# Kernel optimization log

Hardware: AMD Instinct MI355X
Metric: run time of the kernel (lower is better)

Reference implementation:

```python
import jax, jax.numpy as jnp
import numpy as np

B = 4096  # number of rows (batch of 1-D sequences)
N = 4096  # transform length


def setup_inputs() -> dict:
    key = jax.random.key(0)
    x = jax.random.normal(key, (B, N), dtype=jnp.float32)
    # get_expk(N): expk[k] = (cos(pi*k/(2N)), -sin(pi*k/(2N)))
    t = jnp.arange(N, dtype=jnp.float32) * (np.pi / (2.0 * N))
    expk = jnp.stack([jnp.cos(t), -jnp.sin(t)], axis=-1)  # [N, 2]
    return {"x": x, "expk": expk}


def reference(x, expk):
    # IDCT (DCT-III), 2N-point FFT formulation:
    #   y_k = x_0 + 2 * sum_{n=1}^{N-1} x_n cos(pi*n*(2k+1)/(2N))
    #       = Re{ sum_n w_n x_n exp(j*pi*n/(2N)) * exp(j*2*pi*n*k/(2N)) },  w_0=1, w_n=2
    # i.e. the first N outputs of a 2N-point inverse DFT of the zero-padded,
    # twiddle-premultiplied sequence.
    n = x.shape[-1]
    # expk stores (cos(theta), -sin(theta)) => exp(+j*theta) = expk0 - j*expk1
    coef = (expk[..., 0] - 1j * expk[..., 1]).astype(jnp.complex64)  # [N]
    w = jnp.concatenate([jnp.ones((1,), x.dtype), jnp.full((n - 1,), 2.0, x.dtype)])
    a = (x * w).astype(jnp.complex64) * coef                      # [B, N]
    A = jnp.concatenate([a, jnp.zeros_like(a)], axis=-1)          # [B, 2N] zero-pad
    y = jnp.real(jnp.fft.ifft(A, axis=-1))[..., :n] * (2.0 * n)   # undo 1/(2N) of ifft
    return y.astype(x.dtype)
```

## Files before the change

### kernel.cpp

```cpp
#include <hip/hip_runtime.h>


#define NFFT 4096
#define NT   256
#define SWZ(p) ((p) ^ (((p) >> 3) & 0xE))

__device__ __forceinline__ void cmul(float ar, float ai, float br, float bi,
                                     float& orr, float& oii) {
    orr = ar * br - ai * bi;
    oii = ar * bi + ai * br;
}

__device__ __forceinline__ void dft16(float vr[16], float vi[16]) {
    constexpr float WR[4][4] = {
        {1.f, 1.f, 1.f, 1.f},
        {1.f,  0.92387953251128674f,  0.70710678118654752f,  0.38268343236508977f},
        {1.f,  0.70710678118654752f,  0.f,                  -0.70710678118654752f},
        {1.f,  0.38268343236508977f, -0.70710678118654752f, -0.92387953251128674f}};
    constexpr float WI[4][4] = {
        {0.f, 0.f, 0.f, 0.f},
        {0.f,  0.38268343236508977f,  0.70710678118654752f,  0.92387953251128674f},
        {0.f,  0.70710678118654752f,  1.f,                   0.70710678118654752f},
        {0.f,  0.92387953251128674f,  0.70710678118654752f, -0.38268343236508977f}};
    float ur[16], ui[16];
#pragma unroll
    for (int p = 0; p < 4; ++p) {
        float apcr = vr[p] + vr[p + 8],      apci = vi[p] + vi[p + 8];
        float amcr = vr[p] - vr[p + 8],      amci = vi[p] - vi[p + 8];
        float bpdr = vr[p + 4] + vr[p + 12], bpdi = vi[p + 4] + vi[p + 12];
        float bmdr = vr[p + 4] - vr[p + 12], bmdi = vi[p + 4] - vi[p + 12];
        float y0r = apcr + bpdr, y0i = apci + bpdi;
        float y1r = amcr - bmdi, y1i = amci + bmdr;
        float y2r = apcr - bpdr, y2i = apci - bpdi;
        float y3r = amcr + bmdi, y3i = amci - bmdr;
        ur[4 * p + 0] = y0r;  ui[4 * p + 0] = y0i;
        cmul(y1r, y1i, WR[p][1], WI[p][1], ur[4 * p + 1], ui[4 * p + 1]);
        cmul(y2r, y2i, WR[p][2], WI[p][2], ur[4 * p + 2], ui[4 * p + 2]);
        cmul(y3r, y3i, WR[p][3], WI[p][3], ur[4 * p + 3], ui[4 * p + 3]);
    }
#pragma unroll
    for (int q = 0; q < 4; ++q) {
        float apcr = ur[q] + ur[q + 8],      apci = ui[q] + ui[q + 8];
        float amcr = ur[q] - ur[q + 8],      amci = ui[q] - ui[q + 8];
        float bpdr = ur[q + 4] + ur[q + 12], bpdi = ui[q + 4] + ui[q + 12];
        float bmdr = ur[q + 4] - ur[q + 12], bmdi = ui[q + 4] - ui[q + 12];
        vr[q]      = apcr + bpdr;  vi[q]      = apci + bpdi;
        vr[q + 4]  = amcr - bmdi;  vi[q + 4]  = amci + bmdr;
        vr[q + 8]  = apcr - bpdr;  vi[q + 8]  = apci - bpdi;
        vr[q + 12] = amcr + bmdi;  vi[q + 12] = amci - bmdr;
    }
}

__device__ __forceinline__ void twiddle_apply(float vr[16], float vi[16],
                                              float w1r, float w1i) {
    float cr = w1r, ci = w1i;
#pragma unroll
    for (int r = 1; r < 16; ++r) {
        float tr, ti;
        cmul(vr[r], vi[r], cr, ci, tr, ti);
        vr[r] = tr; vi[r] = ti;
        if (r < 15) {
            float nr, ni;
            cmul(cr, ci, w1r, w1i, nr, ni);
            cr = nr; ci = ni;
        }
    }
}

extern "C" __global__ void __launch_bounds__(NT, 5)
idct_fft_kernel(const float* __restrict__ x, const float* __restrict__ expk,
                float* __restrict__ out)
{
    __shared__ __align__(16) float2 S[NFFT];
    float* __restrict__ Sf = (float*)S;

    const int tid = threadIdx.x;
    const long row = blockIdx.x;
    const float* __restrict__ xrow = x + row * (long)NFFT;
    const float2* __restrict__ e2 = (const float2*)expk;

    float vr[16], vi[16];
#pragma unroll
    for (int j = 0; j < 16; ++j) {
        int n = tid + NT * j;
        float xv = xrow[n];
        float2 e = e2[n];
        float w = (n == 0) ? 1.0f : 2.0f;
        vr[j] = w * xv * e.x;
        vi[j] = -(w * xv * e.y);
    }
    dft16(vr, vi);
    {
        float2 we = e2[4 * tid];
        twiddle_apply(vr, vi, we.x, -we.y);
    }
#pragma unroll
    for (int rp = 0; rp < 8; ++rp) {
        int p = 16 * tid + 2 * rp;
        float4 st = make_float4(vr[2 * rp], vi[2 * rp], vr[2 * rp + 1], vi[2 * rp + 1]);
        *(float4*)&S[SWZ(p)] = st;
    }
    __syncthreads();

#pragma unroll
    for (int j = 0; j < 16; ++j) {
        float2 c = S[SWZ(tid + NT * j)];
        vr[j] = c.x; vi[j] = c.y;
    }
    __syncthreads();
    dft16(vr, vi);
    {
        float2 we = e2[64 * (tid >> 4)];
        twiddle_apply(vr, vi, we.x, -we.y);
    }
    {
        int ba = (tid & 15) + ((tid >> 4) << 8);
#pragma unroll
        for (int r = 0; r < 16; ++r) {
            S[SWZ(ba + 16 * r)] = make_float2(vr[r], vi[r]);
        }
    }
    __syncthreads();

#pragma unroll
    for (int j = 0; j < 16; ++j) {
        float2 c = S[SWZ(tid + NT * j)];
        vr[j] = c.x; vi[j] = c.y;
    }
    __syncthreads();
    dft16(vr, vi);
#pragma unroll
    for (int r = 0; r < 16; ++r) {
        Sf[tid + NT * r] = vr[r];
    }
    __syncthreads();

    float2* __restrict__ y2 = (float2*)(out + row * (long)NFFT);
#pragma unroll
    for (int t = 0; t < 8; ++t) {
        int m = tid + NT * t;
        float a = Sf[m];
        float b = Sf[NFFT - 1 - m];
        y2[m] = make_float2(a, b);
    }
}

extern "C" void kernel_launch(void* const* d_in, const int* in_sizes, int n_in,
                              void* d_out, int out_size, void* d_ws, size_t ws_size,
                              hipStream_t stream) {
    const float* x    = (const float*)d_in[0];
    const float* expk = (const float*)d_in[1];
    float* out        = (float*)d_out;
    const int nrows   = in_sizes[0] / NFFT;
    hipLaunchKernelGGL(idct_fft_kernel, dim3(nrows), dim3(NT), 0, stream,
                       x, expk, out);
}
```

Before: 144.4 us.

## Compute IDCT with half-length complex FFT using real-input symmetry

Replaces the 4096-point complex FFT per row with a 2048-point complex FFT. Each input is built from x[k], x[k+M] and their mirrored counterparts using a Hermitian split with extra twiddles, and the stages become radix 16x8x16. Threads per block drop from 256 to 128 and shared memory is halved, and outputs are written as float4 by interleaving the even and odd results. This roughly halves the FFT arithmetic and LDS traffic, at the cost of more complex pre-processing, more global loads per element, and fewer threads per block.

```diff
diff --git a/kernel.cpp b/kernel.cpp
--- a/kernel.cpp
+++ b/kernel.cpp
@@ -1,9 +1,10 @@
 #include <hip/hip_runtime.h>
 
 
-#define NFFT 4096
-#define NT   256
-#define SWZ(p) ((p) ^ (((p) >> 3) & 0xE))
+#define NROW 4096
+#define M    2048
+#define NT   128
+#define SWZ2(a) ((a) ^ ((((a) >> 4) & 7) << 1))
 
 __device__ __forceinline__ void cmul(float ar, float ai, float br, float bi,
                                      float& orr, float& oii) {
@@ -51,6 +52,38 @@
     }
 }
 
+__device__ __forceinline__ void dft4(float& ar, float& ai, float& br, float& bi,
+                                     float& cr, float& ci, float& dr, float& di) {
+    float s02r = ar + cr, s02i = ai + ci;
+    float d02r = ar - cr, d02i = ai - ci;
+    float s13r = br + dr, s13i = bi + di;
+    float d13r = br - dr, d13i = bi - di;
+    ar = s02r + s13r; ai = s02i + s13i;
+    br = d02r - d13i; bi = d02i + d13r;
+    cr = s02r - s13r; ci = s02i - s13i;
+    dr = d02r + d13i; di = d02i - d13r;
+}
+
+__device__ __forceinline__ void dft8(float* vr, float* vi) {
+    float er[4]  = {vr[0], vr[2], vr[4], vr[6]};
+    float ei[4]  = {vi[0], vi[2], vi[4], vi[6]};
+    float odr[4] = {vr[1], vr[3], vr[5], vr[7]};
+    float odi[4] = {vi[1], vi[3], vi[5], vi[7]};
+    dft4(er[0], ei[0], er[1], ei[1], er[2], ei[2], er[3], ei[3]);
+    dft4(odr[0], odi[0], odr[1], odi[1], odr[2], odi[2], odr[3], odi[3]);
+    const float s = 0.70710678118654752f;
+    vr[0] = er[0] + odr[0];            vi[0] = ei[0] + odi[0];
+    vr[4] = er[0] - odr[0];            vi[4] = ei[0] - odi[0];
+    float t1r = s * (odr[1] - odi[1]), t1i = s * (odr[1] + odi[1]);
+    vr[1] = er[1] + t1r;               vi[1] = ei[1] + t1i;
+    vr[5] = er[1] - t1r;               vi[5] = ei[1] - t1i;
+    vr[2] = er[2] - odi[2];            vi[2] = ei[2] + odr[2];
+    vr[6] = er[2] + odi[2];            vi[6] = ei[2] - odr[2];
+    float t3r = -s * (odr[3] + odi[3]), t3i = s * (odr[3] - odi[3]);
+    vr[3] = er[3] + t3r;               vi[3] = ei[3] + t3i;
+    vr[7] = er[3] - t3r;               vi[7] = ei[3] - t3i;
+}
+
 __device__ __forceinline__ void twiddle_apply(float vr[16], float vi[16],
                                               float w1r, float w1i) {
     float cr = w1r, ci = w1i;
@@ -59,89 +92,115 @@
         float tr, ti;
         cmul(vr[r], vi[r], cr, ci, tr, ti);
         vr[r] = tr; vi[r] = ti;
-        if (r < 15) {
-            float nr, ni;
-            cmul(cr, ci, w1r, w1i, nr, ni);
-            cr = nr; ci = ni;
-        }
-    }
-}
-
-extern "C" __global__ void __launch_bounds__(NT, 5)
+        if (r < 15) { float nr, ni; cmul(cr, ci, w1r, w1i, nr, ni); cr = nr; ci = ni; }
+    }
+}
+
+__device__ __forceinline__ void twiddle_apply8(float* vr, float* vi,
+                                               float w1r, float w1i) {
+    float cr = w1r, ci = w1i;
+#pragma unroll
+    for (int r = 1; r < 8; ++r) {
+        float tr, ti;
+        cmul(vr[r], vi[r], cr, ci, tr, ti);
+        vr[r] = tr; vi[r] = ti;
+        if (r < 7) { float nr, ni; cmul(cr, ci, w1r, w1i, nr, ni); cr = nr; ci = ni; }
+    }
+}
+
+extern "C" __global__ void __launch_bounds__(NT, 2)
 idct_fft_kernel(const float* __restrict__ x, const float* __restrict__ expk,
                 float* __restrict__ out)
 {
-    __shared__ __align__(16) float2 S[NFFT];
-    float* __restrict__ Sf = (float*)S;
-
+    __shared__ __align__(16) float2 S[M];
     const int tid = threadIdx.x;
     const long row = blockIdx.x;
-    const float* __restrict__ xrow = x + row * (long)NFFT;
+    const float* __restrict__ xp = x + row * (long)NROW;
     const float2* __restrict__ e2 = (const float2*)expk;
 
     float vr[16], vi[16];
+
 #pragma unroll
     for (int j = 0; j < 16; ++j) {
-        int n = tid + NT * j;
-        float xv = xrow[n];
-        float2 e = e2[n];
-        float w = (n == 0) ? 1.0f : 2.0f;
-        vr[j] = w * xv * e.x;
-        vi[j] = -(w * xv * e.y);
+        int k = tid + NT * j;
+        float x1  = xp[k];
+        float x2  = xp[k + M];
+        float xr1 = (k == 0) ? 0.0f : xp[NROW - k];
+        float xr2 = xp[M - k];
+        float2 E1 = e2[k];
+        float2 E2 = e2[k + M];
+        float c1 = E1.x, s1 = -E1.y;
+        float c2 = E2.x, s2 = -E2.y;
+        float h1r = c1 * x1 + s1 * xr1, h1i = s1 * x1 - c1 * xr1;
+        float h2r = c2 * x2 + s2 * xr2, h2i = s2 * x2 - c2 * xr2;
+        int hi = (k >= 1024);
+        float2 EW = e2[(4 * k) & (NROW - 1)];
+        float wr = hi ? EW.y : EW.x;
+        float wi = hi ? EW.x : -EW.y;
+        float Sr = h1r + h2r, Si = h1i + h2i;
+        float Dr = h1r - h2r, Di = h1i - h2i;
+        vr[j] = Sr - (wr * Di + wi * Dr);
+        vi[j] = Si + (wr * Dr - wi * Di);
     }
     dft16(vr, vi);
+    { float2 E = e2[8 * tid]; twiddle_apply(vr, vi, E.x, -E.y); }
+#pragma unroll
+    for (int rp = 0; rp < 8; ++rp) {
+        int a = 16 * tid + 2 * rp;
+        *(float4*)&S[SWZ2(a)] =
+            make_float4(vr[2 * rp], vi[2 * rp], vr[2 * rp + 1], vi[2 * rp + 1]);
+    }
+    __syncthreads();
+
+    const int p2 = tid & 15, t0a = tid >> 4;
+#pragma unroll
+    for (int h = 0; h < 2; ++h) {
+        int t0 = t0a + 8 * h;
+#pragma unroll
+        for (int t1 = 0; t1 < 8; ++t1) {
+            float2 c = S[SWZ2(16 * t0 + 256 * t1 + p2)];
+            vr[8 * h + t1] = c.x; vi[8 * h + t1] = c.y;
+        }
+    }
+    __syncthreads();
+    dft8(vr, vi);
+    dft8(vr + 8, vi + 8);
+    { float2 E = e2[128 * t0a];       twiddle_apply8(vr, vi, E.x, -E.y); }
+    { float2 E = e2[128 * (t0a + 8)]; twiddle_apply8(vr + 8, vi + 8, E.x, -E.y); }
+#pragma unroll
+    for (int h = 0; h < 2; ++h) {
+        int t0 = t0a + 8 * h;
+#pragma unroll
+        for (int q0 = 0; q0 < 8; ++q0) {
+            S[SWZ2(t0 + 16 * p2 + 256 * q0)] = make_float2(vr[8 * h + q0], vi[8 * h + q0]);
+        }
+    }
+    __syncthreads();
+
+    const int p3 = tid & 15, q03 = tid >> 4;
     {
-        float2 we = e2[4 * tid];
-        twiddle_apply(vr, vi, we.x, -we.y);
-    }
-#pragma unroll
-    for (int rp = 0; rp < 8; ++rp) {
-        int p = 16 * tid + 2 * rp;
-        float4 st = make_float4(vr[2 * rp], vi[2 * rp], vr[2 * rp + 1], vi[2 * rp + 1]);
-        *(float4*)&S[SWZ(p)] = st;
-    }
-    __syncthreads();
-
-#pragma unroll
-    for (int j = 0; j < 16; ++j) {
-        float2 c = S[SWZ(tid + NT * j)];
-        vr[j] = c.x; vi[j] = c.y;
+        int base = 16 * p3 + 256 * q03;
+#pragma unroll
+        for (int tp = 0; tp < 8; ++tp) {
+            float4 c = *(const float4*)&S[SWZ2(base + 2 * tp)];
+            vr[2 * tp] = c.x; vi[2 * tp] = c.y; vr[2 * tp + 1] = c.z; vi[2 * tp + 1] = c.w;
+        }
     }
     __syncthreads();
     dft16(vr, vi);
-    {
-        float2 we = e2[64 * (tid >> 4)];
-        twiddle_apply(vr, vi, we.x, -we.y);
-    }
-    {
-        int ba = (tid & 15) + ((tid >> 4) << 8);
-#pragma unroll
-        for (int r = 0; r < 16; ++r) {
-            S[SWZ(ba + 16 * r)] = make_float2(vr[r], vi[r]);
-        }
-    }
-    __syncthreads();
-
-#pragma unroll
-    for (int j = 0; j < 16; ++j) {
-        float2 c = S[SWZ(tid + NT * j)];
-        vr[j] = c.x; vi[j] = c.y;
-    }
-    __syncthreads();
-    dft16(vr, vi);
-#pragma unroll
-    for (int r = 0; r < 16; ++r) {
-        Sf[tid + NT * r] = vr[r];
-    }
-    __syncthreads();
-
-    float2* __restrict__ y2 = (float2*)(out + row * (long)NFFT);
-#pragma unroll
-    for (int t = 0; t < 8; ++t) {
-        int m = tid + NT * t;
-        float a = Sf[m];
-        float b = Sf[NFFT - 1 - m];
-        y2[m] = make_float2(a, b);
+#pragma unroll
+    for (int q1 = 0; q1 < 16; ++q1) {
+        S[SWZ2(tid + 128 * q1)] = make_float2(vr[q1], vi[q1]);
+    }
+    __syncthreads();
+
+    float4* __restrict__ y4 = (float4*)(out + row * (long)NROW);
+#pragma unroll
+    for (int v = 0; v < 8; ++v) {
+        int u = tid + NT * v;
+        float2 zu = S[SWZ2(u)];
+        float2 zv = S[SWZ2(M - 1 - u)];
+        y4[u] = make_float4(zu.x, zv.y, zu.y, zv.x);
     }
 }
 
@@ -151,7 +210,7 @@
     const float* x    = (const float*)d_in[0];
     const float* expk = (const float*)d_in[1];
     float* out        = (float*)d_out;
-    const int nrows   = in_sizes[0] / NFFT;
+    const int nrows   = in_sizes[0] / NROW;
     hipLaunchKernelGGL(idct_fft_kernel, dim3(nrows), dim3(NT), 0, stream,
                        x, expk, out);
 }
```

After: 137.0 us. -5.1%, faster.
